# Optimization experiments

Measured on AMD Instinct MI355X. Metric: run time of the kernel, lower is better.

Reference implementation:

```python
import jax, jax.numpy as jnp
import numpy as np

B, N, K, H, G, C, P = 2, 8192, 16, 128, 256, 10, 8


def _w(key, fan_in, fan_out):
    return jax.random.normal(key, (fan_in, fan_out), jnp.float32) * (1.0 / np.sqrt(fan_in))


def setup_inputs() -> dict:
    key = jax.random.key(0)
    ks = jax.random.split(key, 24)
    inp = {
        "points": jax.random.normal(ks[0], (B, N, 3), jnp.float32),
        "normals": jax.random.normal(ks[1], (B, N, 3), jnp.float32),
        # point_encoder: Linear(6,H) -> ReLU -> Linear(H,H) -> ReLU
        "We1": _w(ks[2], 6, H), "be1": jnp.zeros((H,), jnp.float32),
        "We2": _w(ks[3], H, H), "be2": jnp.zeros((H,), jnp.float32),
        # local_mlp: Linear(2H,H) -> ReLU -> Linear(H,H) -> ReLU
        "Wl1": _w(ks[4], 2 * H, H), "bl1": jnp.zeros((H,), jnp.float32),
        "Wl2": _w(ks[5], H, H), "bl2": jnp.zeros((H,), jnp.float32),
        # context_proj: Linear(2H,G) -> ReLU
        "Wc": _w(ks[6], 2 * H, G), "bc": jnp.zeros((G,), jnp.float32),
        # classifier: Linear(2H+G,H) -> ReLU -> Linear(H,C)
        "Wk1": _w(ks[7], 2 * H + G, H), "bk1": jnp.zeros((H,), jnp.float32),
        "Wk2": _w(ks[8], H, C), "bk2": jnp.zeros((C,), jnp.float32),
        # param_head: Linear(2H+G,H) -> ReLU -> Linear(H,P)
        "Wp1": _w(ks[9], 2 * H + G, H), "bp1": jnp.zeros((H,), jnp.float32),
        "Wp2": _w(ks[10], H, P), "bp2": jnp.zeros((P,), jnp.float32),
        "k": K,
    }
    return inp


def _knn_indices(points, k):
    # squared pairwise distances (same ordering as torch.cdist); no grad needed
    pts = jax.lax.stop_gradient(points)
    sq = jnp.sum(pts * pts, axis=-1)                      # [B,N]
    d2 = sq[:, :, None] + sq[:, None, :] - 2.0 * jnp.einsum('bnc,bmc->bnm', pts, pts)
    _, idx = jax.lax.top_k(-d2, k + 1)                    # smallest k+1 distances
    return idx[:, :, 1:]                                  # drop self -> [B,N,k]


def _forward(points, normals, We1, be1, We2, be2, Wl1, bl1, Wl2, bl2,
             Wc, bc, Wk1, bk1, Wk2, bk2, Wp1, bp1, Wp2, bp2, k):
    x = jnp.concatenate([points, normals], axis=-1)       # [B,N,6]
    pf = jax.nn.relu(jax.nn.relu(x @ We1 + be1) @ We2 + be2)   # [B,N,H]

    idx = _knn_indices(points, k)                         # [B,N,k]
    nbr = jax.vmap(lambda f, i: f[i])(pf, idx)            # [B,N,k,H]
    ctr = pf[:, :, None, :]
    edge = jnp.concatenate([jnp.broadcast_to(ctr, nbr.shape), nbr - ctr], axis=-1)  # [B,N,k,2H]
    lf = jax.nn.relu(jax.nn.relu(edge @ Wl1 + bl1) @ Wl2 + bl2)
    lf = jnp.max(lf, axis=2)                              # [B,N,H]

    ctx = jax.nn.relu(jnp.concatenate([pf, lf], axis=-1) @ Wc + bc)  # [B,N,G]
    gf = jnp.max(ctx, axis=1, keepdims=True)              # [B,1,G]
    gf = jnp.broadcast_to(gf, (pf.shape[0], pf.shape[1], gf.shape[-1]))

    fused = jnp.concatenate([pf, lf, gf], axis=-1)        # [B,N,2H+G]
    logits = jax.nn.relu(fused @ Wk1 + bk1) @ Wk2 + bk2
    param_pred = jax.nn.relu(fused @ Wp1 + bp1) @ Wp2 + bp2
    return logits, param_pred


def reference(points, normals, We1, be1, We2, be2, Wl1, bl1, Wl2, bl2,
              Wc, bc, Wk1, bk1, Wk2, bk2, Wp1, bp1, Wp2, bp2, k):
    return _forward(points, normals, We1, be1, We2, be2, Wl1, bl1, Wl2, bl2,
                    Wc, bc, Wk1, bk1, Wk2, bk2, Wp1, bp1, Wp2, bp2, k)
```

## Files before the change

### kernel.cpp

```cpp
#include <hip/hip_runtime.h>

#define B_ 2
#define N_ 8192
#define NP 16384
#define K_ 16
#define H_ 128
#define KCAP 512

typedef short bf16x8 __attribute__((ext_vector_type(8)));
typedef float f32x4 __attribute__((ext_vector_type(4)));

__device__ inline unsigned short f2b(float f) {
    unsigned u = __builtin_bit_cast(unsigned, f);
    unsigned r = (u + 0x7fff + ((u >> 16) & 1)) >> 16;
    return (unsigned short)r;
}
__device__ inline bf16x8 ldb8(const unsigned short* p) {
    return *(const bf16x8*)p;
}
__device__ inline uint4 pack8(float4 a, float4 b) {
    uint4 pk;
    pk.x = (unsigned)f2b(a.x) | ((unsigned)f2b(a.y) << 16);
    pk.y = (unsigned)f2b(a.z) | ((unsigned)f2b(a.w) << 16);
    pk.z = (unsigned)f2b(b.x) | ((unsigned)f2b(b.y) << 16);
    pk.w = (unsigned)f2b(b.z) | ((unsigned)f2b(b.w) << 16);
    return pk;
}

__global__ __launch_bounds__(256) void k_pf(
    const float* __restrict__ pts, const float* __restrict__ nrm,
    const float* __restrict__ We1, const float* __restrict__ be1,
    const float* __restrict__ We2, const float* __restrict__ be2,
    float* __restrict__ pf, float* __restrict__ gf, float4* __restrict__ pts4) {
    __shared__ float w2s[128 * 128];
    __shared__ float w1s[6 * 128];
    __shared__ float b1s[128], b2s[128];
    __shared__ float xs[2][6];
    __shared__ float h1s[2][128];
    int t = threadIdx.x;
    for (int i = t; i < 128 * 128; i += 256) w2s[i] = We2[i];
    for (int i = t; i < 6 * 128; i += 256) w1s[i] = We1[i];
    if (t < 128) { b1s[t] = be1[t]; b2s[t] = be2[t]; }
    if (blockIdx.x == 0) { gf[t] = 0.f; gf[256 + t] = 0.f; }
    int base = blockIdx.x * 64;
    if (t < 64) {
        int p = base + t;
        float x = pts[p * 3], y = pts[p * 3 + 1], z = pts[p * 3 + 2];
        float sq = __fadd_rn(__fadd_rn(__fmul_rn(x, x), __fmul_rn(y, y)), __fmul_rn(z, z));
        pts4[p] = make_float4(x, y, z, sq);
    }
    __syncthreads();
    int g = t >> 7, h = t & 127;
    for (int it = 0; it < 32; ++it) {
        int p = base + it * 2 + g;
        if (h < 3) xs[g][h] = pts[p * 3 + h];
        else if (h < 6) xs[g][h] = nrm[p * 3 + h - 3];
        __syncthreads();
        float a = b1s[h];
        #pragma unroll
        for (int c = 0; c < 6; ++c) a += xs[g][c] * w1s[c * 128 + h];
        h1s[g][h] = fmaxf(a, 0.f);
        __syncthreads();
        float o = b2s[h];
        #pragma unroll 8
        for (int c = 0; c < 128; ++c) o += h1s[g][c] * w2s[c * 128 + h];
        pf[p * 128 + h] = fmaxf(o, 0.f);
        __syncthreads();
    }
}

__global__ __launch_bounds__(256) void k_prep(
    const float* __restrict__ Wl1, const float* __restrict__ bl1,
    const float* __restrict__ Wl2, const float* __restrict__ Wc,
    const float* __restrict__ Wk1, const float* __restrict__ Wp1,
    unsigned short* __restrict__ WuvT, float* __restrict__ bias_cat,
    unsigned short* __restrict__ Wl2T, unsigned short* __restrict__ WcT,
    unsigned short* __restrict__ Wk1T, unsigned short* __restrict__ Wp1T) {
    int tid = blockIdx.x * 256 + threadIdx.x;
    int stride = gridDim.x * 256;
    for (int i = tid; i < 256 * 128; i += stride) {
        int n = i >> 7, k = i & 127;
        float val = (n < 128) ? Wl1[k * 128 + n] - Wl1[(k + 128) * 128 + n]
                              : Wl1[(k + 128) * 128 + (n - 128)];
        WuvT[i] = f2b(val);
    }
    for (int i = tid; i < 256; i += stride) bias_cat[i] = (i < 128) ? bl1[i] : 0.f;
    for (int i = tid; i < 128 * 128; i += stride) {
        int n = i >> 7, k = i & 127;
        Wl2T[i] = f2b(Wl2[k * 128 + n]);
    }
    for (int i = tid; i < 256 * 256; i += stride) {
        int n = i >> 8, k = i & 255;
        WcT[i] = f2b(Wc[k * 256 + n]);
    }
    for (int i = tid; i < 128 * 512; i += stride) {
        int n = i >> 9, k = i & 511;
        Wk1T[i] = f2b(Wk1[k * 128 + n]);
        Wp1T[i] = f2b(Wp1[k * 128 + n]);
    }
}

__global__ __launch_bounds__(256) void k_knn(
    const float4* __restrict__ pts4, int* __restrict__ knn) {
    __shared__ int hist[4][260];
    __shared__ unsigned long long buf[4][KCAP];
    int t = threadIdx.x, w = t >> 6, l = t & 63;
    int b = blockIdx.x >> 11;
    int q = (blockIdx.x & 2047) * 4 + w;
    const float4* pb = pts4 + b * N_;
    float4 qp = pb[q];
    for (int i = l; i < 256; i += 64) hist[w][i] = 0;
    int cntw = 0;

    #pragma unroll 2
    for (int i = 0; i < 16; ++i) {
        int j = l + 64 * i;
        float4 c = pb[j];
        float dot = __fadd_rn(__fadd_rn(__fmul_rn(qp.x, c.x), __fmul_rn(qp.y, c.y)), __fmul_rn(qp.z, c.z));
        float d2 = __fsub_rn(__fadd_rn(qp.w, c.w), __fmul_rn(2.f, dot));
        d2 = (j == q) ? 1e30f : d2;
        unsigned uu = __float_as_uint(d2);
        int bk = (d2 < 0.f) ? 0 : min(255, max(0, (int)(uu >> 21) - 400));
        atomicAdd(&hist[w][bk], 1);
    }
    float Tf;
    {
        int h0 = hist[w][4 * l], h1 = hist[w][4 * l + 1], h2 = hist[w][4 * l + 2], h3 = hist[w][4 * l + 3];
        int c0 = h0, c1 = c0 + h1, c2 = c1 + h2, c3 = c2 + h3;
        int tot = c3;
        int inc = tot;
        for (int off = 1; off < 64; off <<= 1) {
            int vv = __shfl_up(inc, off);
            if (l >= off) inc += vv;
        }
        int excl = inc - tot;
        int Bc = 255;
        if      (excl + c0 >= 16) Bc = 4 * l;
        else if (excl + c1 >= 16) Bc = 4 * l + 1;
        else if (excl + c2 >= 16) Bc = 4 * l + 2;
        else if (excl + c3 >= 16) Bc = 4 * l + 3;
        for (int m = 1; m < 64; m <<= 1) Bc = min(Bc, __shfl_xor(Bc, m));
        Tf = __uint_as_float((unsigned)(Bc + 401) << 21);
    }

    #pragma unroll 4
    for (int i = 0; i < 128; ++i) {
        int j = l + 64 * i;
        float4 c = pb[j];
        float dot = __fadd_rn(__fadd_rn(__fmul_rn(qp.x, c.x), __fmul_rn(qp.y, c.y)), __fmul_rn(qp.z, c.z));
        float d2 = __fsub_rn(__fadd_rn(qp.w, c.w), __fmul_rn(2.f, dot));
        bool take = (d2 < Tf);
        unsigned long long mask = __ballot(take);
        if (take) {
            unsigned du = __float_as_uint(d2);
            unsigned mu = du ^ (unsigned)(((int)du >> 31) | 0x80000000);
            int pos = cntw + __popcll(mask & ((1ull << l) - 1ull));
            if (pos < KCAP) buf[w][pos] = ((unsigned long long)mu << 32) | (unsigned)j;
        }
        cntw += __popcll(mask);
    }
    int m_ = min(cntw, KCAP);

    unsigned long long key[8];
    #pragma unroll
    for (int r = 0; r < 8; ++r) {
        int e = l + 64 * r;
        key[r] = (e < m_) ? buf[w][e] : ~0ull;
    }
    int emitted = 0;
    for (int r17 = 0; r17 < 17 && emitted < 16; ++r17) {
        unsigned long long mn = key[0];
        #pragma unroll
        for (int r = 1; r < 8; ++r) mn = (key[r] < mn) ? key[r] : mn;
        unsigned long long wv = mn;
        for (int m = 1; m < 64; m <<= 1) {
            unsigned long long o = __shfl_xor(wv, m);
            wv = (o < wv) ? o : wv;
        }
        int idx = (int)(wv & 0xffffffffu);
        if (idx != q) {
            if (l == 0) knn[((size_t)b * N_ + q) * 16 + emitted] = b * N_ + idx;
            ++emitted;
        }
        #pragma unroll
        for (int r = 0; r < 8; ++r) if (key[r] == wv) key[r] = ~0ull;
    }
}

__global__ __launch_bounds__(256) void k_uv(
    const float* __restrict__ pf, const unsigned short* __restrict__ WuvT,
    const float* __restrict__ bias_cat,
    float* __restrict__ u, float* __restrict__ v) {
    __shared__ __align__(16) unsigned short As[128 * 136];
    int t = threadIdx.x;
    int l = t & 63, w = t >> 6;
    int wr = w >> 1, wcn = w & 1;
    int rowbase = blockIdx.x * 128;
    int ncol0 = blockIdx.y * 128;

    #pragma unroll
    for (int i = 0; i < 8; ++i) {
        int ci = t + 256 * i;
        int r = ci >> 4, c8 = (ci & 15) * 8;
        const float4* sp = (const float4*)(pf + (size_t)(rowbase + r) * 128 + c8);
        *(uint4*)&As[r * 136 + c8] = pack8(sp[0], sp[1]);
    }
    __syncthreads();

    f32x4 acc[4][4];
    #pragma unroll
    for (int i = 0; i < 4; ++i)
        #pragma unroll
        for (int j = 0; j < 4; ++j) acc[i][j] = (f32x4){0.f, 0.f, 0.f, 0.f};

    #pragma unroll
    for (int ks = 0; ks < 4; ++ks) {
        bf16x8 bfr[4], afr[4];
        #pragma unroll
        for (int nj = 0; nj < 4; ++nj)
            bfr[nj] = ldb8(&WuvT[(size_t)(ncol0 + wcn * 64 + nj * 16 + (l & 15)) * 128 + ks * 32 + (l >> 4) * 8]);
        #pragma unroll
        for (int mi = 0; mi < 4; ++mi)
            afr[mi] = ldb8(&As[(wr * 64 + mi * 16 + (l & 15)) * 136 + ks * 32 + (l >> 4) * 8]);
        #pragma unroll
        for (int mi = 0; mi < 4; ++mi)
            #pragma unroll
            for (int nj = 0; nj < 4; ++nj)
                acc[mi][nj] = __builtin_amdgcn_mfma_f32_16x16x32_bf16(afr[mi], bfr[nj], acc[mi][nj], 0, 0, 0);
    }
    float* outp = (ncol0 == 0) ? u : v;
    #pragma unroll
    for (int mi = 0; mi < 4; ++mi)
        #pragma unroll
        for (int nj = 0; nj < 4; ++nj) {
            int col = wcn * 64 + nj * 16 + (l & 15);
            float bias = bias_cat[ncol0 + col];
            #pragma unroll
            for (int rg = 0; rg < 4; ++rg) {
                int row = wr * 64 + mi * 16 + (l >> 4) * 4 + rg;
                outp[(size_t)(rowbase + row) * 128 + col] = acc[mi][nj][rg] + bias;
            }
        }
}

__global__ __launch_bounds__(256) void k_edge(
    const float* __restrict__ u, const float* __restrict__ v,
    const int* __restrict__ knn, const unsigned short* __restrict__ Wl2T,
    const float* __restrict__ bl2, float* __restrict__ lf) {
    __shared__ __align__(16) unsigned short h1s[128 * 136];
    int t = threadIdx.x;
    int l = t & 63, w = t >> 6;
    int wr = w >> 1, wcn = w & 1;
    int rowbase = blockIdx.x * 128;
    int p0 = blockIdx.x * 8;

    #pragma unroll 2
    for (int i = 0; i < 8; ++i) {
        int ci = t + 256 * i;
        int r = ci >> 4, c8 = (ci & 15) * 8;
        int nb = knn[rowbase + r];
        int pt = p0 + (r >> 4);
        const float4* vp = (const float4*)(v + (size_t)nb * 128 + c8);
        const float4* up = (const float4*)(u + (size_t)pt * 128 + c8);
        float4 va = vp[0], vb = vp[1];
        float4 ua = up[0], ub = up[1];
        unsigned d0 = (unsigned)f2b(fmaxf(ua.x + va.x, 0.f)) | ((unsigned)f2b(fmaxf(ua.y + va.y, 0.f)) << 16);
        unsigned d1 = (unsigned)f2b(fmaxf(ua.z + va.z, 0.f)) | ((unsigned)f2b(fmaxf(ua.w + va.w, 0.f)) << 16);
        unsigned d2 = (unsigned)f2b(fmaxf(ub.x + vb.x, 0.f)) | ((unsigned)f2b(fmaxf(ub.y + vb.y, 0.f)) << 16);
        unsigned d3 = (unsigned)f2b(fmaxf(ub.z + vb.z, 0.f)) | ((unsigned)f2b(fmaxf(ub.w + vb.w, 0.f)) << 16);
        uint4 pk; pk.x = d0; pk.y = d1; pk.z = d2; pk.w = d3;
        *(uint4*)&h1s[r * 136 + c8] = pk;
    }
    __syncthreads();

    f32x4 acc[4][4];
    #pragma unroll
    for (int i = 0; i < 4; ++i)
        #pragma unroll
        for (int j = 0; j < 4; ++j) acc[i][j] = (f32x4){0.f, 0.f, 0.f, 0.f};

    #pragma unroll
    for (int ks = 0; ks < 4; ++ks) {
        bf16x8 bfr[4], afr[4];
        #pragma unroll
        for (int nj = 0; nj < 4; ++nj)
            bfr[nj] = ldb8(&Wl2T[(size_t)(wcn * 64 + nj * 16 + (l & 15)) * 128 + ks * 32 + (l >> 4) * 8]);
        #pragma unroll
        for (int mi = 0; mi < 4; ++mi)
            afr[mi] = ldb8(&h1s[(wr * 64 + mi * 16 + (l & 15)) * 136 + ks * 32 + (l >> 4) * 8]);
        #pragma unroll
        for (int mi = 0; mi < 4; ++mi)
            #pragma unroll
            for (int nj = 0; nj < 4; ++nj)
                acc[mi][nj] = __builtin_amdgcn_mfma_f32_16x16x32_bf16(afr[mi], bfr[nj], acc[mi][nj], 0, 0, 0);
    }

    #pragma unroll
    for (int mi = 0; mi < 4; ++mi)
        #pragma unroll
        for (int nj = 0; nj < 4; ++nj) {
            int col = wcn * 64 + nj * 16 + (l & 15);
            float bias = bl2[col];
            float m = fmaxf(acc[mi][nj][0] + bias, 0.f);
            m = fmaxf(m, fmaxf(acc[mi][nj][1] + bias, 0.f));
            m = fmaxf(m, fmaxf(acc[mi][nj][2] + bias, 0.f));
            m = fmaxf(m, fmaxf(acc[mi][nj][3] + bias, 0.f));
            m = fmaxf(m, __shfl_xor(m, 16));
            m = fmaxf(m, __shfl_xor(m, 32));
            if (l < 16) lf[(size_t)(p0 + wr * 4 + mi) * 128 + col] = m;
        }
}

__global__ __launch_bounds__(256) void k_ctx(
    const float* __restrict__ pf, const float* __restrict__ lf,
    const unsigned short* __restrict__ WcT, const float* __restrict__ bc,
    float* __restrict__ gf) {
    __shared__ __align__(16) unsigned short As[128 * 136];
    int t = threadIdx.x;
    int l = t & 63, w = t >> 6;
    int wr = w >> 1, wcn = w & 1;
    int rowbase = blockIdx.x * 128;
    int ncol0 = blockIdx.y * 128;
    int b = rowbase >> 13;

    f32x4 acc[4][4];
    #pragma unroll
    for (int i = 0; i < 4; ++i)
        #pragma unroll
        for (int j = 0; j < 4; ++j) acc[i][j] = (f32x4){0.f, 0.f, 0.f, 0.f};

    for (int kb = 0; kb < 2; ++kb) {
        const float* src = kb ? lf : pf;
        #pragma unroll
        for (int i = 0; i < 8; ++i) {
            int ci = t + 256 * i;
            int r = ci >> 4, c8 = (ci & 15) * 8;
            const float4* sp = (const float4*)(src + (size_t)(rowbase + r) * 128 + c8);
            *(uint4*)&As[r * 136 + c8] = pack8(sp[0], sp[1]);
        }
        __syncthreads();
        #pragma unroll
        for (int ks = 0; ks < 4; ++ks) {
            bf16x8 bfr[4], afr[4];
            #pragma unroll
            for (int nj = 0; nj < 4; ++nj)
                bfr[nj] = ldb8(&WcT[(size_t)(ncol0 + wcn * 64 + nj * 16 + (l & 15)) * 256 + kb * 128 + ks * 32 + (l >> 4) * 8]);
            #pragma unroll
            for (int mi = 0; mi < 4; ++mi)
                afr[mi] = ldb8(&As[(wr * 64 + mi * 16 + (l & 15)) * 136 + ks * 32 + (l >> 4) * 8]);
            #pragma unroll
            for (int mi = 0; mi < 4; ++mi)
                #pragma unroll
                for (int nj = 0; nj < 4; ++nj)
                    acc[mi][nj] = __builtin_amdgcn_mfma_f32_16x16x32_bf16(afr[mi], bfr[nj], acc[mi][nj], 0, 0, 0);
        }
        __syncthreads();
    }
    #pragma unroll
    for (int nj = 0; nj < 4; ++nj) {
        int col = ncol0 + wcn * 64 + nj * 16 + (l & 15);
        float m = acc[0][nj][0];
        #pragma unroll
        for (int mi = 0; mi < 4; ++mi)
            #pragma unroll
            for (int rg = 0; rg < 4; ++rg) m = fmaxf(m, acc[mi][nj][rg]);
        m = fmaxf(m + bc[col], 0.f);
        m = fmaxf(m, __shfl_xor(m, 16));
        m = fmaxf(m, __shfl_xor(m, 32));
        if (l < 16) atomicMax((unsigned int*)&gf[b * 256 + col], __float_as_uint(m));
    }
}

__global__ __launch_bounds__(256) void k_head(
    const float* __restrict__ pf, const float* __restrict__ lf, const float* __restrict__ gf,
    const unsigned short* __restrict__ Wk1T, const float* __restrict__ bk1,
    const float* __restrict__ Wk2, const float* __restrict__ bk2,
    const unsigned short* __restrict__ Wp1T, const float* __restrict__ bp1,
    const float* __restrict__ Wp2, const float* __restrict__ bp2,
    float* __restrict__ out) {
    __shared__ __align__(16) char smem[67584];
    unsigned short* As = (unsigned short*)smem;
    float* hs = (float*)smem;
    int t = threadIdx.x;
    int l = t & 63, w = t >> 6;
    int wr = w >> 1, wcn = w & 1;
    int rowbase = blockIdx.x * 128;
    int b = rowbase >> 13;
    int br = blockIdx.y;
    const unsigned short* W1T = br ? Wp1T : Wk1T;
    const float* b1 = br ? bp1 : bk1;
    const float* W2 = br ? Wp2 : Wk2;
    const float* b2p = br ? bp2 : bk2;
    int OC = br ? 8 : 10;
    float* obase = out + (br ? (size_t)NP * 10 : 0);

    f32x4 acc[4][4];
    #pragma unroll
    for (int i = 0; i < 4; ++i)
        #pragma unroll
        for (int j = 0; j < 4; ++j) acc[i][j] = (f32x4){0.f, 0.f, 0.f, 0.f};

    for (int kb = 0; kb < 4; ++kb) {
        #pragma unroll
        for (int i = 0; i < 8; ++i) {
            int ci = t + 256 * i;
            int r = ci >> 4, c8 = (ci & 15) * 8;
            const float4* sp;
            if (kb == 0)      sp = (const float4*)(pf + (size_t)(rowbase + r) * 128 + c8);
            else if (kb == 1) sp = (const float4*)(lf + (size_t)(rowbase + r) * 128 + c8);
            else              sp = (const float4*)(gf + b * 256 + (kb - 2) * 128 + c8);
            *(uint4*)&As[r * 136 + c8] = pack8(sp[0], sp[1]);
        }
        __syncthreads();
        #pragma unroll
        for (int ks = 0; ks < 4; ++ks) {
            bf16x8 bfr[4], afr[4];
            #pragma unroll
            for (int nj = 0; nj < 4; ++nj)
                bfr[nj] = ldb8(&W1T[(size_t)(wcn * 64 + nj * 16 + (l & 15)) * 512 + kb * 128 + ks * 32 + (l >> 4) * 8]);
            #pragma unroll
            for (int mi = 0; mi < 4; ++mi)
                afr[mi] = ldb8(&As[(wr * 64 + mi * 16 + (l & 15)) * 136 + ks * 32 + (l >> 4) * 8]);
            #pragma unroll
            for (int mi = 0; mi < 4; ++mi)
                #pragma unroll
                for (int nj = 0; nj < 4; ++nj)
                    acc[mi][nj] = __builtin_amdgcn_mfma_f32_16x16x32_bf16(afr[mi], bfr[nj], acc[mi][nj], 0, 0, 0);
        }
        __syncthreads();
    }
    #pragma unroll
    for (int mi = 0; mi < 4; ++mi)
        #pragma unroll
        for (int nj = 0; nj < 4; ++nj)
            #pragma unroll
            for (int rg = 0; rg < 4; ++rg) {
                int row = wr * 64 + mi * 16 + (l >> 4) * 4 + rg;
                int col = wcn * 64 + nj * 16 + (l & 15);
                hs[row * 132 + col] = fmaxf(acc[mi][nj][rg] + b1[col], 0.f);
            }
    __syncthreads();
    for (int o = t; o < 128 * OC; o += 256) {
        int r = o / OC, c = o % OC;
        float a = b2p[c];
        for (int k2 = 0; k2 < 128; ++k2) a += hs[r * 132 + k2] * W2[k2 * OC + c];
        obase[(size_t)(rowbase + r) * OC + c] = a;
    }
}

extern "C" void kernel_launch(void* const* d_in, const int* in_sizes, int n_in,
                              void* d_out, int out_size, void* d_ws, size_t ws_size,
                              hipStream_t stream) {
    const float* pts = (const float*)d_in[0];
    const float* nrm = (const float*)d_in[1];
    const float* We1 = (const float*)d_in[2];
    const float* be1 = (const float*)d_in[3];
    const float* We2 = (const float*)d_in[4];
    const float* be2 = (const float*)d_in[5];
    const float* Wl1 = (const float*)d_in[6];
    const float* bl1 = (const float*)d_in[7];
    const float* Wl2 = (const float*)d_in[8];
    const float* bl2 = (const float*)d_in[9];
    const float* Wc  = (const float*)d_in[10];
    const float* bc  = (const float*)d_in[11];
    const float* Wk1 = (const float*)d_in[12];
    const float* bk1 = (const float*)d_in[13];
    const float* Wk2 = (const float*)d_in[14];
    const float* bk2 = (const float*)d_in[15];
    const float* Wp1 = (const float*)d_in[16];
    const float* bp1 = (const float*)d_in[17];
    const float* Wp2 = (const float*)d_in[18];
    const float* bp2 = (const float*)d_in[19];
    float* out = (float*)d_out;

    char* ws = (char*)d_ws;
    size_t off = 0;
    float* pf = (float*)(ws + off);       off += (size_t)NP * 128 * 4;
    float* lf = (float*)(ws + off);       off += (size_t)NP * 128 * 4;
    float* u  = (float*)(ws + off);       off += (size_t)NP * 128 * 4;
    float* v  = (float*)(ws + off);       off += (size_t)NP * 128 * 4;
    int* knn  = (int*)(ws + off);         off += (size_t)NP * 16 * 4;
    float* gf = (float*)(ws + off);       off += 2048;
    float4* pts4 = (float4*)(ws + off);   off += (size_t)NP * 16;
    float* bias_cat = (float*)(ws + off); off += 1024;
    unsigned short* WuvT = (unsigned short*)(ws + off); off += 256 * 128 * 2;
    unsigned short* Wl2T = (unsigned short*)(ws + off); off += 128 * 128 * 2;
    unsigned short* WcT  = (unsigned short*)(ws + off); off += 256 * 256 * 2;
    unsigned short* Wk1T = (unsigned short*)(ws + off); off += 128 * 512 * 2;
    unsigned short* Wp1T = (unsigned short*)(ws + off); off += 128 * 512 * 2;

    hipLaunchKernelGGL(k_pf, dim3(256), dim3(256), 0, stream,
                       pts, nrm, We1, be1, We2, be2, pf, gf, pts4);
    hipLaunchKernelGGL(k_prep, dim3(64), dim3(256), 0, stream,
                       Wl1, bl1, Wl2, Wc, Wk1, Wp1,
                       WuvT, bias_cat, Wl2T, WcT, Wk1T, Wp1T);
    hipLaunchKernelGGL(k_knn, dim3(4096), dim3(256), 0, stream, pts4, knn);
    hipLaunchKernelGGL(k_uv, dim3(128, 2), dim3(256), 0, stream,
                       pf, WuvT, bias_cat, u, v);
    hipLaunchKernelGGL(k_edge, dim3(2048), dim3(256), 0, stream,
                       u, v, knn, Wl2T, bl2, lf);
    hipLaunchKernelGGL(k_ctx, dim3(128, 2), dim3(256), 0, stream,
                       pf, lf, WcT, bc, gf);
    hipLaunchKernelGGL(k_head, dim3(128, 2), dim3(256), 0, stream,
                       pf, lf, gf, Wk1T, bk1, Wk2, bk2, Wp1T, bp1, Wp2, bp2, out);
}
```

Baseline: 391.1 us.

## Split point encoder into bf16 MFMA GEMM and process two kNN queries per wave

The fused scalar point-encoder kernel becomes two kernels. An elementwise kernel writes the first layer in bf16, and an MFMA kernel computes the 128x128 second layer from a bf16-transposed We2 prepared in k_prep. The kNN kernel now handles two queries per wave so each candidate point load is shared. It caches the first 16 distance chunks in registers and stores only indices in the candidate buffer, recomputing distances at selection time. The selection loop rescans a lane's keys only when that lane supplied the winning key. The costs are bf16 rounding in the encoder's second layer and higher register pressure in kNN.

```diff
diff --git a/kernel.cpp b/kernel.cpp
--- a/kernel.cpp
+++ b/kernel.cpp
@@ -27,45 +27,29 @@
     return pk;
 }
 
-__global__ __launch_bounds__(256) void k_pf(
+__global__ __launch_bounds__(256) void k_h1(
     const float* __restrict__ pts, const float* __restrict__ nrm,
     const float* __restrict__ We1, const float* __restrict__ be1,
-    const float* __restrict__ We2, const float* __restrict__ be2,
-    float* __restrict__ pf, float* __restrict__ gf, float4* __restrict__ pts4) {
-    __shared__ float w2s[128 * 128];
-    __shared__ float w1s[6 * 128];
-    __shared__ float b1s[128], b2s[128];
-    __shared__ float xs[2][6];
-    __shared__ float h1s[2][128];
-    int t = threadIdx.x;
-    for (int i = t; i < 128 * 128; i += 256) w2s[i] = We2[i];
-    for (int i = t; i < 6 * 128; i += 256) w1s[i] = We1[i];
-    if (t < 128) { b1s[t] = be1[t]; b2s[t] = be2[t]; }
-    if (blockIdx.x == 0) { gf[t] = 0.f; gf[256 + t] = 0.f; }
-    int base = blockIdx.x * 64;
-    if (t < 64) {
-        int p = base + t;
+    unsigned short* __restrict__ h1, float* __restrict__ gf,
+    float4* __restrict__ pts4) {
+    int tid = blockIdx.x * 256 + threadIdx.x;
+    if (blockIdx.x == 0) { gf[threadIdx.x] = 0.f; gf[256 + threadIdx.x] = 0.f; }
+    if (tid < NP) {
+        int p = tid;
         float x = pts[p * 3], y = pts[p * 3 + 1], z = pts[p * 3 + 2];
         float sq = __fadd_rn(__fadd_rn(__fmul_rn(x, x), __fmul_rn(y, y)), __fmul_rn(z, z));
         pts4[p] = make_float4(x, y, z, sq);
     }
-    __syncthreads();
-    int g = t >> 7, h = t & 127;
-    for (int it = 0; it < 32; ++it) {
-        int p = base + it * 2 + g;
-        if (h < 3) xs[g][h] = pts[p * 3 + h];
-        else if (h < 6) xs[g][h] = nrm[p * 3 + h - 3];
-        __syncthreads();
-        float a = b1s[h];
-        #pragma unroll
-        for (int c = 0; c < 6; ++c) a += xs[g][c] * w1s[c * 128 + h];
-        h1s[g][h] = fmaxf(a, 0.f);
-        __syncthreads();
-        float o = b2s[h];
-        #pragma unroll 8
-        for (int c = 0; c < 128; ++c) o += h1s[g][c] * w2s[c * 128 + h];
-        pf[p * 128 + h] = fmaxf(o, 0.f);
-        __syncthreads();
+    for (int o = tid; o < NP * 128; o += gridDim.x * 256) {
+        int p = o >> 7, h = o & 127;
+        float a = be1[h];
+        a += pts[p * 3]     * We1[0 * 128 + h];
+        a += pts[p * 3 + 1] * We1[1 * 128 + h];
+        a += pts[p * 3 + 2] * We1[2 * 128 + h];
+        a += nrm[p * 3]     * We1[3 * 128 + h];
+        a += nrm[p * 3 + 1] * We1[4 * 128 + h];
+        a += nrm[p * 3 + 2] * We1[5 * 128 + h];
+        h1[o] = f2b(fmaxf(a, 0.f));
     }
 }
 
@@ -73,9 +57,11 @@
     const float* __restrict__ Wl1, const float* __restrict__ bl1,
     const float* __restrict__ Wl2, const float* __restrict__ Wc,
     const float* __restrict__ Wk1, const float* __restrict__ Wp1,
+    const float* __restrict__ We2,
     unsigned short* __restrict__ WuvT, float* __restrict__ bias_cat,
     unsigned short* __restrict__ Wl2T, unsigned short* __restrict__ WcT,
-    unsigned short* __restrict__ Wk1T, unsigned short* __restrict__ Wp1T) {
+    unsigned short* __restrict__ Wk1T, unsigned short* __restrict__ Wp1T,
+    unsigned short* __restrict__ We2T) {
     int tid = blockIdx.x * 256 + threadIdx.x;
     int stride = gridDim.x * 256;
     for (int i = tid; i < 256 * 128; i += stride) {
@@ -88,6 +74,7 @@
     for (int i = tid; i < 128 * 128; i += stride) {
         int n = i >> 7, k = i & 127;
         Wl2T[i] = f2b(Wl2[k * 128 + n]);
+        We2T[i] = f2b(We2[k * 128 + n]);
     }
     for (int i = tid; i < 256 * 256; i += stride) {
         int n = i >> 8, k = i & 255;
@@ -100,90 +87,173 @@
     }
 }
 
+__global__ __launch_bounds__(256) void k_pf2(
+    const unsigned short* __restrict__ h1, const unsigned short* __restrict__ We2T,
+    const float* __restrict__ be2, float* __restrict__ pf) {
+    int t = threadIdx.x, l = t & 63, w = t >> 6;
+    int row0 = blockIdx.x * 64 + w * 16;
+    f32x4 acc[8];
+    #pragma unroll
+    for (int nj = 0; nj < 8; ++nj) acc[nj] = (f32x4){0.f, 0.f, 0.f, 0.f};
+    #pragma unroll
+    for (int ks = 0; ks < 4; ++ks) {
+        bf16x8 a = ldb8(&h1[(size_t)(row0 + (l & 15)) * 128 + ks * 32 + (l >> 4) * 8]);
+        #pragma unroll
+        for (int nj = 0; nj < 8; ++nj) {
+            bf16x8 bfr = ldb8(&We2T[(size_t)(nj * 16 + (l & 15)) * 128 + ks * 32 + (l >> 4) * 8]);
+            acc[nj] = __builtin_amdgcn_mfma_f32_16x16x32_bf16(a, bfr, acc[nj], 0, 0, 0);
+        }
+    }
+    #pragma unroll
+    for (int nj = 0; nj < 8; ++nj) {
+        int col = nj * 16 + (l & 15);
+        float bias = be2[col];
+        #pragma unroll
+        for (int rg = 0; rg < 4; ++rg) {
+            int row = row0 + (l >> 4) * 4 + rg;
+            pf[(size_t)row * 128 + col] = fmaxf(acc[nj][rg] + bias, 0.f);
+        }
+    }
+}
+
+__device__ inline float knn_thresh(const int* __restrict__ hh, int l) {
+    int h0 = hh[4 * l], h1 = hh[4 * l + 1], h2 = hh[4 * l + 2], h3 = hh[4 * l + 3];
+    int c0 = h0, c1 = c0 + h1, c2 = c1 + h2, c3 = c2 + h3;
+    int tot = c3;
+    int inc = tot;
+    for (int off = 1; off < 64; off <<= 1) {
+        int vv = __shfl_up(inc, off);
+        if (l >= off) inc += vv;
+    }
+    int excl = inc - tot;
+    int Bc = 255;
+    if      (excl + c0 >= 16) Bc = 4 * l;
+    else if (excl + c1 >= 16) Bc = 4 * l + 1;
+    else if (excl + c2 >= 16) Bc = 4 * l + 2;
+    else if (excl + c3 >= 16) Bc = 4 * l + 3;
+    for (int m = 1; m < 64; m <<= 1) Bc = min(Bc, __shfl_xor(Bc, m));
+    return __uint_as_float((unsigned)(Bc + 401) << 21);
+}
+
 __global__ __launch_bounds__(256) void k_knn(
     const float4* __restrict__ pts4, int* __restrict__ knn) {
-    __shared__ int hist[4][260];
-    __shared__ unsigned long long buf[4][KCAP];
+    __shared__ int hist[4][2][260];
+    __shared__ unsigned buf[4][2][KCAP];
     int t = threadIdx.x, w = t >> 6, l = t & 63;
-    int b = blockIdx.x >> 11;
-    int q = (blockIdx.x & 2047) * 4 + w;
+    int b = blockIdx.x >> 10;
+    int qbase = (blockIdx.x & 1023) * 8 + w * 2;
     const float4* pb = pts4 + b * N_;
-    float4 qp = pb[q];
-    for (int i = l; i < 256; i += 64) hist[w][i] = 0;
-    int cntw = 0;
-
-    #pragma unroll 2
+    float4 qp0 = pb[qbase];
+    float4 qp1 = pb[qbase + 1];
+    for (int i = l; i < 520; i += 64) (&hist[w][0][0])[i] = 0;
+    int cnt0 = 0, cnt1 = 0;
+
+    float d2c0[16], d2c1[16];
+    #pragma unroll
     for (int i = 0; i < 16; ++i) {
         int j = l + 64 * i;
         float4 c = pb[j];
-        float dot = __fadd_rn(__fadd_rn(__fmul_rn(qp.x, c.x), __fmul_rn(qp.y, c.y)), __fmul_rn(qp.z, c.z));
-        float d2 = __fsub_rn(__fadd_rn(qp.w, c.w), __fmul_rn(2.f, dot));
-        d2 = (j == q) ? 1e30f : d2;
-        unsigned uu = __float_as_uint(d2);
-        int bk = (d2 < 0.f) ? 0 : min(255, max(0, (int)(uu >> 21) - 400));
-        atomicAdd(&hist[w][bk], 1);
-    }
-    float Tf;
-    {
-        int h0 = hist[w][4 * l], h1 = hist[w][4 * l + 1], h2 = hist[w][4 * l + 2], h3 = hist[w][4 * l + 3];
-        int c0 = h0, c1 = c0 + h1, c2 = c1 + h2, c3 = c2 + h3;
-        int tot = c3;
-        int inc = tot;
-        for (int off = 1; off < 64; off <<= 1) {
-            int vv = __shfl_up(inc, off);
-            if (l >= off) inc += vv;
-        }
-        int excl = inc - tot;
-        int Bc = 255;
-        if      (excl + c0 >= 16) Bc = 4 * l;
-        else if (excl + c1 >= 16) Bc = 4 * l + 1;
-        else if (excl + c2 >= 16) Bc = 4 * l + 2;
-        else if (excl + c3 >= 16) Bc = 4 * l + 3;
-        for (int m = 1; m < 64; m <<= 1) Bc = min(Bc, __shfl_xor(Bc, m));
-        Tf = __uint_as_float((unsigned)(Bc + 401) << 21);
-    }
-
-    #pragma unroll 4
-    for (int i = 0; i < 128; ++i) {
+        float dot0 = __fadd_rn(__fadd_rn(__fmul_rn(qp0.x, c.x), __fmul_rn(qp0.y, c.y)), __fmul_rn(qp0.z, c.z));
+        float d20 = __fsub_rn(__fadd_rn(qp0.w, c.w), __fmul_rn(2.f, dot0));
+        float dot1 = __fadd_rn(__fadd_rn(__fmul_rn(qp1.x, c.x), __fmul_rn(qp1.y, c.y)), __fmul_rn(qp1.z, c.z));
+        float d21 = __fsub_rn(__fadd_rn(qp1.w, c.w), __fmul_rn(2.f, dot1));
+        d2c0[i] = d20; d2c1[i] = d21;
+        float hv0 = (j == qbase) ? 1e30f : d20;
+        float hv1 = (j == qbase + 1) ? 1e30f : d21;
+        unsigned u0 = __float_as_uint(hv0);
+        int bk0 = (hv0 < 0.f) ? 0 : min(255, max(0, (int)(u0 >> 21) - 400));
+        atomicAdd(&hist[w][0][bk0], 1);
+        unsigned u1 = __float_as_uint(hv1);
+        int bk1 = (hv1 < 0.f) ? 0 : min(255, max(0, (int)(u1 >> 21) - 400));
+        atomicAdd(&hist[w][1][bk1], 1);
+    }
+    float Tf0 = knn_thresh(&hist[w][0][0], l);
+    float Tf1 = knn_thresh(&hist[w][1][0], l);
+
+    #pragma unroll
+    for (int i = 0; i < 16; ++i) {
+        int j = l + 64 * i;
+        bool t0 = d2c0[i] < Tf0;
+        unsigned long long m0 = __ballot(t0);
+        if (t0) {
+            int pos = cnt0 + __popcll(m0 & ((1ull << l) - 1ull));
+            if (pos < KCAP) buf[w][0][pos] = (unsigned)j;
+        }
+        cnt0 += __popcll(m0);
+        bool t1 = d2c1[i] < Tf1;
+        unsigned long long m1 = __ballot(t1);
+        if (t1) {
+            int pos = cnt1 + __popcll(m1 & ((1ull << l) - 1ull));
+            if (pos < KCAP) buf[w][1][pos] = (unsigned)j;
+        }
+        cnt1 += __popcll(m1);
+    }
+
+    #pragma unroll 2
+    for (int i = 16; i < 128; ++i) {
         int j = l + 64 * i;
         float4 c = pb[j];
-        float dot = __fadd_rn(__fadd_rn(__fmul_rn(qp.x, c.x), __fmul_rn(qp.y, c.y)), __fmul_rn(qp.z, c.z));
-        float d2 = __fsub_rn(__fadd_rn(qp.w, c.w), __fmul_rn(2.f, dot));
-        bool take = (d2 < Tf);
-        unsigned long long mask = __ballot(take);
-        if (take) {
-            unsigned du = __float_as_uint(d2);
-            unsigned mu = du ^ (unsigned)(((int)du >> 31) | 0x80000000);
-            int pos = cntw + __popcll(mask & ((1ull << l) - 1ull));
-            if (pos < KCAP) buf[w][pos] = ((unsigned long long)mu << 32) | (unsigned)j;
-        }
-        cntw += __popcll(mask);
-    }
-    int m_ = min(cntw, KCAP);
-
-    unsigned long long key[8];
-    #pragma unroll
-    for (int r = 0; r < 8; ++r) {
-        int e = l + 64 * r;
-        key[r] = (e < m_) ? buf[w][e] : ~0ull;
-    }
-    int emitted = 0;
-    for (int r17 = 0; r17 < 17 && emitted < 16; ++r17) {
-        unsigned long long mn = key[0];
-        #pragma unroll
-        for (int r = 1; r < 8; ++r) mn = (key[r] < mn) ? key[r] : mn;
-        unsigned long long wv = mn;
-        for (int m = 1; m < 64; m <<= 1) {
-            unsigned long long o = __shfl_xor(wv, m);
-            wv = (o < wv) ? o : wv;
-        }
-        int idx = (int)(wv & 0xffffffffu);
-        if (idx != q) {
-            if (l == 0) knn[((size_t)b * N_ + q) * 16 + emitted] = b * N_ + idx;
-            ++emitted;
-        }
-        #pragma unroll
-        for (int r = 0; r < 8; ++r) if (key[r] == wv) key[r] = ~0ull;
+        float dot0 = __fadd_rn(__fadd_rn(__fmul_rn(qp0.x, c.x), __fmul_rn(qp0.y, c.y)), __fmul_rn(qp0.z, c.z));
+        float d20 = __fsub_rn(__fadd_rn(qp0.w, c.w), __fmul_rn(2.f, dot0));
+        float dot1 = __fadd_rn(__fadd_rn(__fmul_rn(qp1.x, c.x), __fmul_rn(qp1.y, c.y)), __fmul_rn(qp1.z, c.z));
+        float d21 = __fsub_rn(__fadd_rn(qp1.w, c.w), __fmul_rn(2.f, dot1));
+        bool t0 = d20 < Tf0;
+        unsigned long long m0 = __ballot(t0);
+        if (t0) {
+            int pos = cnt0 + __popcll(m0 & ((1ull << l) - 1ull));
+            if (pos < KCAP) buf[w][0][pos] = (unsigned)j;
+        }
+        cnt0 += __popcll(m0);
+        bool t1 = d21 < Tf1;
+        unsigned long long m1 = __ballot(t1);
+        if (t1) {
+            int pos = cnt1 + __popcll(m1 & ((1ull << l) - 1ull));
+            if (pos < KCAP) buf[w][1][pos] = (unsigned)j;
+        }
+        cnt1 += __popcll(m1);
+    }
+
+    for (int qq = 0; qq < 2; ++qq) {
+        int q = qbase + qq;
+        float4 qp = qq ? qp1 : qp0;
+        int m_ = min(qq ? cnt1 : cnt0, KCAP);
+        unsigned long long key[8];
+        #pragma unroll
+        for (int r = 0; r < 8; ++r) {
+            int e = l + 64 * r;
+            if (e < m_) {
+                int idx = (int)buf[w][qq][e];
+                float4 c = pb[idx];
+                float dot = __fadd_rn(__fadd_rn(__fmul_rn(qp.x, c.x), __fmul_rn(qp.y, c.y)), __fmul_rn(qp.z, c.z));
+                float d2 = __fsub_rn(__fadd_rn(qp.w, c.w), __fmul_rn(2.f, dot));
+                unsigned du = __float_as_uint(d2);
+                unsigned mu = du ^ (unsigned)(((int)du >> 31) | 0x80000000);
+                key[r] = ((unsigned long long)mu << 32) | (unsigned)idx;
+            } else key[r] = ~0ull;
+        }
+        unsigned long long lmin = key[0];
+        #pragma unroll
+        for (int r = 1; r < 8; ++r) lmin = (key[r] < lmin) ? key[r] : lmin;
+        int emitted = 0;
+        for (int r17 = 0; r17 < 17 && emitted < 16; ++r17) {
+            unsigned long long wv = lmin;
+            for (int m = 1; m < 64; m <<= 1) {
+                unsigned long long o = __shfl_xor(wv, m);
+                wv = (o < wv) ? o : wv;
+            }
+            int idx = (int)(wv & 0xffffffffu);
+            if (idx != q) {
+                if (l == 0) knn[((size_t)b * N_ + q) * 16 + emitted] = b * N_ + idx;
+                ++emitted;
+            }
+            if (lmin == wv) {
+                #pragma unroll
+                for (int r = 0; r < 8; ++r) if (key[r] == wv) key[r] = ~0ull;
+                lmin = key[0];
+                #pragma unroll
+                for (int r = 1; r < 8; ++r) lmin = (key[r] < lmin) ? key[r] : lmin;
+            }
+        }
     }
 }
 
@@ -488,13 +558,17 @@
     unsigned short* WcT  = (unsigned short*)(ws + off); off += 256 * 256 * 2;
     unsigned short* Wk1T = (unsigned short*)(ws + off); off += 128 * 512 * 2;
     unsigned short* Wp1T = (unsigned short*)(ws + off); off += 128 * 512 * 2;
-
-    hipLaunchKernelGGL(k_pf, dim3(256), dim3(256), 0, stream,
-                       pts, nrm, We1, be1, We2, be2, pf, gf, pts4);
+    unsigned short* We2T = (unsigned short*)(ws + off); off += 128 * 128 * 2;
+    unsigned short* h1   = (unsigned short*)(ws + off); off += (size_t)NP * 128 * 2;
+
+    hipLaunchKernelGGL(k_h1, dim3(2048), dim3(256), 0, stream,
+                       pts, nrm, We1, be1, h1, gf, pts4);
     hipLaunchKernelGGL(k_prep, dim3(64), dim3(256), 0, stream,
-                       Wl1, bl1, Wl2, Wc, Wk1, Wp1,
-                       WuvT, bias_cat, Wl2T, WcT, Wk1T, Wp1T);
-    hipLaunchKernelGGL(k_knn, dim3(4096), dim3(256), 0, stream, pts4, knn);
+                       Wl1, bl1, Wl2, Wc, Wk1, Wp1, We2,
+                       WuvT, bias_cat, Wl2T, WcT, Wk1T, Wp1T, We2T);
+    hipLaunchKernelGGL(k_knn, dim3(2048), dim3(256), 0, stream, pts4, knn);
+    hipLaunchKernelGGL(k_pf2, dim3(256), dim3(256), 0, stream,
+                       h1, We2T, be2, pf);
     hipLaunchKernelGGL(k_uv, dim3(128, 2), dim3(256), 0, stream,
                        pf, WuvT, bias_cat, u, v);
     hipLaunchKernelGGL(k_edge, dim3(2048), dim3(256), 0, stream,
```

Measured after the change: 358.0 us. -8.4%, faster.
